# Kernel tuning notes

Measured on AMD Instinct MI355X. Metric: run time of the kernel, lower is better.

## Reference

```python
import jax, jax.numpy as jnp
import numpy as np

B, T, W, HP = 1, 64, 88, 48   # batch, frames, pitches, hidden_per_pitch
NU, NH, K = 24, 4, 25          # n_unit, n_heads, neighborhood window
HD = NU // NH                  # head dim = 6
HL = NU // 2                   # LSTM hidden per direction = 12


def _lstm_bidir(x, w_ih, w_hh, b_ih, b_hh):
    # x: [N, T, In]; w_ih: [2, 4*HL, In]; w_hh: [2, 4*HL, HL]; biases: [2, 4*HL]
    N = x.shape[0]
    def run(Wih, Whh, bih, bhh, reverse):
        def step(carry, xt):
            h, c = carry
            g = xt @ Wih.T + h @ Whh.T + bih + bhh
            i, f, gg, o = jnp.split(g, 4, axis=-1)  # torch gate order i,f,g,o
            c = jax.nn.sigmoid(f) * c + jax.nn.sigmoid(i) * jnp.tanh(gg)
            h = jax.nn.sigmoid(o) * jnp.tanh(c)
            return (h, c), h
        init = (jnp.zeros((N, HL), x.dtype), jnp.zeros((N, HL), x.dtype))
        _, ys = jax.lax.scan(step, init, jnp.swapaxes(x, 0, 1), reverse=reverse)
        return jnp.swapaxes(ys, 0, 1)
    return jnp.concatenate([run(w_ih[0], w_hh[0], b_ih[0], b_hh[0], False),
                            run(w_ih[1], w_hh[1], b_ih[1], b_hh[1], True)], axis=-1)


def _natten2d(x, qkv_w, qkv_b, rpb, proj_w, proj_b):
    # Neighborhood attention over 2D grid [B, Hh, Ww] with KxK window clamped at borders.
    Bn, Hh, Ww, C = x.shape
    qkv = (x @ qkv_w.T + qkv_b).reshape(Bn, Hh, Ww, 3, NH, HD)
    q = qkv[..., 0, :, :] * (HD ** -0.5)
    k = qkv[..., 1, :, :]
    v = qkv[..., 2, :, :]
    half = K // 2
    ar = jnp.arange(K)
    idx_i = jnp.clip(jnp.arange(Hh) - half, 0, Hh - K)[:, None] + ar  # [Hh,K]
    idx_j = jnp.clip(jnp.arange(Ww) - half, 0, Ww - K)[:, None] + ar  # [Ww,K]
    kg = k[:, idx_i][:, :, :, idx_j]  # [B,Hh,K,Ww,K,NH,HD]
    vg = v[:, idx_i][:, :, :, idx_j]
    ri = idx_i - jnp.arange(Hh)[:, None] + (K - 1)  # relative pos bias indices [Hh,K]
    rj = idx_j - jnp.arange(Ww)[:, None] + (K - 1)  # [Ww,K]
    bias = rpb[:, ri][:, :, :, rj]                  # [NH,Hh,K,Ww,K]
    logits = jnp.einsum('bijnd,biajcnd->bnijac', q, kg)
    logits = logits + jnp.transpose(bias, (0, 1, 3, 2, 4))[None]
    attn = jax.nn.softmax(logits.reshape(Bn, NH, Hh, Ww, K * K), axis=-1)
    attn = attn.reshape(Bn, NH, Hh, Ww, K, K)
    out = jnp.einsum('bnijac,biajcnd->bijnd', attn, vg).reshape(Bn, Hh, Ww, C)
    return out @ proj_w.T + proj_b


def _forward(features, condition, mask, emb, w_ih_l0, w_hh_l0, b_ih_l0, b_hh_l0,
             w_ih_l1, w_hh_l1, b_ih_l1, b_hh_l1, qkv_w, qkv_b, rpb, proj_w, proj_b,
             out_w, out_b):
    # concat: [B,T,88,HP] + [B,T,88,4] + [B,T,88,1] -> [B,T,88,HP+5]
    cat = jnp.concatenate([jnp.transpose(features, (0, 1, 3, 2)), emb[condition],
                           mask[..., None]], axis=-1)
    x = jnp.transpose(cat, (0, 2, 1, 3)).reshape(B * W, T, HP + 5)  # pitchwise LSTM
    x = _lstm_bidir(x, w_ih_l0, w_hh_l0, b_ih_l0, b_hh_l0)
    x = _lstm_bidir(x, w_ih_l1, w_hh_l1, b_ih_l1, b_hh_l1)
    x = jnp.transpose(x.reshape(B, W, T, NU), (0, 2, 1, 3))  # [B,T,88,NU]
    for _ in range(2):  # n_layers=2; Sequential(*[m]*2) => SHARED weights
        x = _natten2d(x, qkv_w, qkv_b, rpb, proj_w, proj_b)
    return x @ out_w.T + out_b  # [B,T,88,5]


def setup_inputs():
    ks = jax.random.split(jax.random.key(0), 24)
    def unif(k, shape, fan):
        s = 1.0 / np.sqrt(fan)
        return jax.random.uniform(k, shape, jnp.float32, -s, s)
    return {
        'features': jax.random.normal(ks[0], (B, T, HP, W), jnp.float32),
        'condition': jax.random.randint(ks[1], (B, T, W), 0, 5),
        'mask': jax.random.uniform(ks[2], (B, T, W), jnp.float32),
        'emb': jax.random.normal(ks[3], (5, 4), jnp.float32),
        'w_ih_l0': unif(ks[4], (2, 4 * HL, HP + 5), HL),
        'w_hh_l0': unif(ks[5], (2, 4 * HL, HL), HL),
        'b_ih_l0': unif(ks[6], (2, 4 * HL), HL),
        'b_hh_l0': unif(ks[7], (2, 4 * HL), HL),
        'w_ih_l1': unif(ks[8], (2, 4 * HL, 2 * HL), HL),
        'w_hh_l1': unif(ks[9], (2, 4 * HL, HL), HL),
        'b_ih_l1': unif(ks[10], (2, 4 * HL), HL),
        'b_hh_l1': unif(ks[11], (2, 4 * HL), HL),
        'qkv_w': unif(ks[12], (3 * NU, NU), NU),
        'qkv_b': unif(ks[13], (3 * NU,), NU),
        'rpb': jax.random.normal(ks[14], (NH, 2 * K - 1, 2 * K - 1), jnp.float32) * 0.02,
        'proj_w': unif(ks[15], (NU, NU), NU),
        'proj_b': unif(ks[16], (NU,), NU),
        'out_w': unif(ks[17], (5, NU), NU),
        'out_b': unif(ks[18], (5,), NU),
    }


def reference(features, condition, mask, emb, w_ih_l0, w_hh_l0, b_ih_l0, b_hh_l0,
              w_ih_l1, w_hh_l1, b_ih_l1, b_hh_l1, qkv_w, qkv_b, rpb, proj_w, proj_b,
              out_w, out_b):
    return _forward(features, condition, mask, emb, w_ih_l0, w_hh_l0, b_ih_l0, b_hh_l0,
                    w_ih_l1, w_hh_l1, b_ih_l1, b_hh_l1, qkv_w, qkv_b, rpb,
                    proj_w, proj_b, out_w, out_b)
```

## Files before the change

### kernel.cpp

```cpp
#include <hip/hip_runtime.h>
#include <hip/hip_bf16.h>

#define NPIX (64*88)
#define NSEQ 88
#define TT 64
#define F0 53
#define GATES 48

typedef __hip_bfloat16 bf16;

__device__ __forceinline__ float frcp(float x){ return __builtin_amdgcn_rcpf(x); }
__device__ __forceinline__ float blo(unsigned u){ return __uint_as_float(u<<16); }
__device__ __forceinline__ float bhi(unsigned u){ return __uint_as_float(u & 0xffff0000u); }

__global__ __launch_bounds__(1024) void k_core(
    const float* __restrict__ feat, const int* __restrict__ cond,
    const float* __restrict__ mask, const float* __restrict__ emb,
    const float* __restrict__ wih0, const float* __restrict__ whh0,
    const float* __restrict__ bih0, const float* __restrict__ bhh0,
    const float* __restrict__ wih1, const float* __restrict__ whh1,
    const float* __restrict__ bih1, const float* __restrict__ bhh1,
    const float* __restrict__ qkv_w, const float* __restrict__ qkv_b,
    float* __restrict__ q, bf16* __restrict__ kh, bf16* __restrict__ vh){
  int n = (blockIdx.x & 7)*11 + (blockIdx.x >> 3);
  int tid = threadIdx.x;
  int wave = tid >> 6; int lane = tid & 63;
  __shared__ float smem[14816];
  float* gbuf = smem;
  float* sx   = smem + 6144;
  float* sw0  = smem + 6144+3392;
  float* w1   = smem + 6144;
  float* sqkv = smem + 6144+2400;
  float* y0   = smem + 6144+4200;
  float* y1   = smem + 6144+5736;
  float* bsum = smem + 14624;

  for (int idx = tid; idx < 2*GATES*F0; idx += 1024) sw0[idx] = wih0[idx];
  for (int idx = tid; idx < TT*F0; idx += 1024){
    int t = idx / F0, f = idx - t*F0;
    float v;
    if (f < 48)      v = feat[(t*48 + f)*88 + n];
    else if (f < 52) v = emb[cond[t*88+n]*4 + (f-48)];
    else             v = mask[t*88+n];
    sx[idx] = v;
  }
  if (tid < 96)       bsum[tid] = bih0[tid] + bhh0[tid];
  else if (tid < 192) bsum[tid] = bih1[tid-96] + bhh1[tid-96];
  __syncthreads();

  #pragma unroll
  for (int r = 0; r < 6; ++r){
    int row = tid + r*1024;
    int d = row / 3072; int rem = row - d*3072;
    int t = rem / 48; int j = rem - t*48;
    const float* xr = sx + t*F0;
    const float* wr = sw0 + (d*GATES + j)*F0;
    float a0=0.f, a1=0.f, a2=0.f, a3=0.f;
    #pragma unroll
    for (int f=0; f<52; f+=4){
      a0 += xr[f  ]*wr[f  ];
      a1 += xr[f+1]*wr[f+1];
      a2 += xr[f+2]*wr[f+2];
      a3 += xr[f+3]*wr[f+3];
    }
    gbuf[(d*TT + t)*GATES + j] = bsum[d*GATES+j] + xr[52]*wr[52] + ((a0+a1)+(a2+a3));
  }
  __syncthreads();

  if (wave >= 2){
    for (int idx = tid-128; idx < 2*GATES*24; idx += 896){
      int row = idx / 24, f = idx - row*24;
      w1[row*25 + f] = wih1[idx];
    }
    for (int idx = tid-128; idx < 72*24; idx += 896){
      int row = idx / 24, f = idx - row*24;
      sqkv[row*25 + f] = qkv_w[idx];
    }
  } else {
    int d = wave;
    int j = (lane < GATES) ? lane : (lane - GATES);
    int u = j % 12; int grp = j / 12;
    float w[12];
    const float* wb = whh0 + (d*GATES + j)*12;
    #pragma unroll
    for (int m=0;m<12;++m) w[m] = wb[m];
    float negs  = (grp==2) ? -2.f : -1.f;
    float amul  = (grp==2) ?  2.f :  1.f;
    float aadd  = (grp==2) ? -1.f :  0.f;
    const float* gb = gbuf + d*TT*GATES + j;
    float hval = 0.f, cval = 0.f;
    int t0 = d ? (TT-1) : 0;
    float gnext = gb[t0*GATES];
    for (int s=0;s<TT;++s){
      int t = d ? (TT-1-s) : s;
      float gg = gnext;
      int tn = d ? max(TT-2-s,0) : min(s+1,TT-1);
      gnext = gb[tn*GATES];
      float h0=__shfl(hval,0), h1=__shfl(hval,1), h2=__shfl(hval,2);
      float h3=__shfl(hval,3), h4=__shfl(hval,4), h5=__shfl(hval,5);
      float h6=__shfl(hval,6), h7=__shfl(hval,7), h8=__shfl(hval,8);
      float h9=__shfl(hval,9), h10=__shfl(hval,10), h11=__shfl(hval,11);
      float a0 = gg + h0*w[0] + h4*w[4] + h8*w[8];
      float a1 = h1*w[1] + h5*w[5] + h9*w[9];
      float a2 = h2*w[2] + h6*w[6] + h10*w[10];
      float a3 = h3*w[3] + h7*w[7] + h11*w[11];
      float dot = (a0+a1)+(a2+a3);
      float act = amul*frcp(1.f + __expf(negs*dot)) + aadd;
      float ai = __shfl(act, u);
      float af = __shfl(act, u+12);
      float ag = __shfl(act, u+24);
      float ao = __shfl(act, u+36);
      float cn = af*cval + ai*ag;
      float th = 2.f*frcp(1.f + __expf(-2.f*cn)) - 1.f;
      hval = ao*th; cval = cn;
      if (lane < 12) y0[t*24 + d*12 + lane] = hval;
    }
  }
  __syncthreads();

  #pragma unroll
  for (int r = 0; r < 6; ++r){
    int row = tid + r*1024;
    int d = row / 3072; int rem = row - d*3072;
    int t = rem / 48; int j = rem - t*48;
    const float* xr = y0 + t*24;
    const float* wr = w1 + (d*GATES + j)*25;
    float a0=0.f, a1=0.f;
    #pragma unroll
    for (int c=0; c<24; c+=2){ a0 += xr[c]*wr[c]; a1 += xr[c+1]*wr[c+1]; }
    gbuf[(d*TT + t)*GATES + j] = bsum[96 + d*GATES+j] + a0 + a1;
  }
  __syncthreads();

  if (wave < 2){
    int d = wave;
    int j = (lane < GATES) ? lane : (lane - GATES);
    int u = j % 12; int grp = j / 12;
    float w[12];
    const float* wb = whh1 + (d*GATES + j)*12;
    #pragma unroll
    for (int m=0;m<12;++m) w[m] = wb[m];
    float negs  = (grp==2) ? -2.f : -1.f;
    float amul  = (grp==2) ?  2.f :  1.f;
    float aadd  = (grp==2) ? -1.f :  0.f;
    const float* gb = gbuf + d*TT*GATES + j;
    float hval = 0.f, cval = 0.f;
    int t0 = d ? (TT-1) : 0;
    float gnext = gb[t0*GATES];
    for (int s=0;s<TT;++s){
      int t = d ? (TT-1-s) : s;
      float gg = gnext;
      int tn = d ? max(TT-2-s,0) : min(s+1,TT-1);
      gnext = gb[tn*GATES];
      float h0=__shfl(hval,0), h1=__shfl(hval,1), h2=__shfl(hval,2);
      float h3=__shfl(hval,3), h4=__shfl(hval,4), h5=__shfl(hval,5);
      float h6=__shfl(hval,6), h7=__shfl(hval,7), h8=__shfl(hval,8);
      float h9=__shfl(hval,9), h10=__shfl(hval,10), h11=__shfl(hval,11);
      float a0 = gg + h0*w[0] + h4*w[4] + h8*w[8];
      float a1 = h1*w[1] + h5*w[5] + h9*w[9];
      float a2 = h2*w[2] + h6*w[6] + h10*w[10];
      float a3 = h3*w[3] + h7*w[7] + h11*w[11];
      float dot = (a0+a1)+(a2+a3);
      float act = amul*frcp(1.f + __expf(negs*dot)) + aadd;
      float ai = __shfl(act, u);
      float af = __shfl(act, u+12);
      float ag = __shfl(act, u+24);
      float ao = __shfl(act, u+36);
      float cn = af*cval + ai*ag;
      float th = 2.f*frcp(1.f + __expf(-2.f*cn)) - 1.f;
      hval = ao*th; cval = cn;
      if (lane < 12) y1[t*24 + d*12 + lane] = hval;
    }
  }
  __syncthreads();

  for (int idx = tid; idx < TT*72; idx += 1024){
    int gq = idx % 72; int t = idx / 72;
    int p = t*88 + n;
    const float* xr = y1 + t*24;
    const float* wr = sqkv + gq*25;
    float a0=0.f, a1=0.f;
    #pragma unroll
    for (int c=0; c<24; c+=2){ a0 += xr[c]*wr[c]; a1 += xr[c+1]*wr[c+1]; }
    float acc = qkv_b[gq] + a0 + a1;
    int s = gq/24, rem = gq - s*24;
    if (s==0) q[p*24+rem] = acc*0.4082482904638631f;
    else {
      int hh = rem/6, pos = rem - hh*6;
      bf16* dst = (s==1) ? kh : vh;
      dst[((size_t)hh*NPIX + p)*8 + pos] = __float2bfloat16(acc);
    }
  }
}

__global__ __launch_bounds__(512) void k_attn(
    const float* __restrict__ q, const bf16* __restrict__ kh,
    const bf16* __restrict__ vh, const float* __restrict__ rpb,
    float* __restrict__ ao){
  int b = blockIdx.x;
  int h = b / 704; int rem = b - h*704;
  int ti = rem / 44, tj = rem - ti*44;
  int i0 = ti*4, j0 = tj*2;
  int tid = threadIdx.x;
  int w = tid >> 6; int lane = tid & 63;
  int osi = min(max(i0-12,0),39);
  int osj = min(max(j0-12,0),63);

  __shared__ unsigned kt[728*5];
  __shared__ unsigned vt[728*5];
  const uint4* kg = (const uint4*)(kh + (size_t)h*NPIX*8);
  const uint4* vg = (const uint4*)(vh + (size_t)h*NPIX*8);
  for (int idx = tid; idx < 728; idx += 512){
    int a = idx / 26, cc = idx - a*26;
    int gi = min(osi + a, 63), gj = min(osj + cc, 87);
    int src = gi*88 + gj;
    uint4 kr = kg[src];
    uint4 vr = vg[src];
    int o = idx*5;
    kt[o] = kr.x; kt[o+1] = kr.y; kt[o+2] = kr.z;
    vt[o] = vr.x; vt[o+1] = vr.y; vt[o+2] = vr.z;
  }
  __syncthreads();

  int pi = i0 + (w>>1), pj = j0 + (w&1);
  int p = pi*88 + pj;
  int dsi = min(max(pi-12,0),39) - osi;
  int dsj = min(max(pj-12,0),63) - osj;
  int rbi = osi + dsi - pi + 24;
  int rbj = osj + dsj - pj + 24;

  float qv[6];
  #pragma unroll
  for (int d=0; d<6; ++d) qv[d] = q[p*24 + h*6 + d];

  float lgv[10]; int rof[10];
  float lmax = -1e30f;
  #pragma unroll
  for (int it=0; it<10; ++it){
    int nb = lane + it*64;
    bool valid = nb < 625;
    int nbc = valid ? nb : 624;
    int a = nbc/25, cc = nbc - a*25;
    int r5 = ((a+dsi)*26 + (cc+dsj))*5;
    rof[it] = r5;
    unsigned k0 = kt[r5], k1 = kt[r5+1], k2 = kt[r5+2];
    float lg = qv[0]*blo(k0)+qv[1]*bhi(k0)+qv[2]*blo(k1)
             + qv[3]*bhi(k1)+qv[4]*blo(k2)+qv[5]*bhi(k2);
    lg += rpb[(h*49 + (a + rbi))*49 + (cc + rbj)];
    lg = valid ? lg : -1e30f;
    lgv[it] = lg;
    lmax = fmaxf(lmax, lg);
  }
  #pragma unroll
  for (int off=32; off; off>>=1) lmax = fmaxf(lmax, __shfl_xor(lmax, off));
  float lsum = 0.f;
  #pragma unroll
  for (int it=0; it<10; ++it){
    float pe = __expf(lgv[it]-lmax);
    lgv[it] = pe; lsum += pe;
  }
  #pragma unroll
  for (int off=32; off; off>>=1) lsum += __shfl_xor(lsum, off);
  float acc[6] = {0,0,0,0,0,0};
  #pragma unroll
  for (int it=0; it<10; ++it){
    int r5 = rof[it];
    unsigned v0 = vt[r5], v1 = vt[r5+1], v2 = vt[r5+2];
    float pe = lgv[it];
    acc[0] += pe*blo(v0); acc[1] += pe*bhi(v0);
    acc[2] += pe*blo(v1); acc[3] += pe*bhi(v1);
    acc[4] += pe*blo(v2); acc[5] += pe*bhi(v2);
  }
  #pragma unroll
  for (int d=0; d<6; ++d){
    #pragma unroll
    for (int off=32; off; off>>=1) acc[d] += __shfl_xor(acc[d], off);
  }
  if (lane == 0){
    float inv = frcp(lsum);
    #pragma unroll
    for (int d=0; d<6; ++d) ao[p*24 + h*6 + d] = acc[d]*inv;
  }
}

__global__ __launch_bounds__(64) void k_proj_qkv(const float* __restrict__ ain,
    const float* __restrict__ pw, const float* __restrict__ pb,
    const float* __restrict__ qkv_w, const float* __restrict__ qkv_b,
    float* __restrict__ q2, bf16* __restrict__ kh2, bf16* __restrict__ vh2){
  int p = blockIdx.x; int tid = threadIdx.x;
  __shared__ float arow[24];
  __shared__ float xrow[24];
  if (tid < 24) arow[tid] = ain[p*24+tid];
  __syncthreads();
  if (tid < 24){
    float a2 = pb[tid];
    const float* wr = pw + tid*24;
    #pragma unroll
    for (int c=0;c<24;++c) a2 += arow[c]*wr[c];
    xrow[tid] = a2;
  }
  __syncthreads();
  for (int g = tid; g < 72; g += 64){
    float a2 = qkv_b[g];
    const float* wr = qkv_w + g*24;
    #pragma unroll
    for (int c=0;c<24;++c) a2 += xrow[c]*wr[c];
    int s = g/24, rem = g - s*24;
    if (s==0) q2[p*24+rem] = a2*0.4082482904638631f;
    else {
      int hh = rem/6, pos = rem - hh*6;
      bf16* dst = (s==1) ? kh2 : vh2;
      dst[((size_t)hh*NPIX + p)*8 + pos] = __float2bfloat16(a2);
    }
  }
}

__global__ __launch_bounds__(64) void k_proj_out(const float* __restrict__ ain,
    const float* __restrict__ pw, const float* __restrict__ pb,
    const float* __restrict__ ow, const float* __restrict__ ob,
    float* __restrict__ out){
  int p = blockIdx.x; int tid = threadIdx.x;
  __shared__ float arow[24];
  __shared__ float xrow[24];
  if (tid < 24) arow[tid] = ain[p*24+tid];
  __syncthreads();
  if (tid < 24){
    float a2 = pb[tid];
    const float* wr = pw + tid*24;
    #pragma unroll
    for (int c=0;c<24;++c) a2 += arow[c]*wr[c];
    xrow[tid] = a2;
  }
  __syncthreads();
  if (tid < 5){
    float a2 = ob[tid];
    const float* wr = ow + tid*24;
    #pragma unroll
    for (int c=0;c<24;++c) a2 += xrow[c]*wr[c];
    out[p*5+tid] = a2;
  }
}

extern "C" void kernel_launch(void* const* d_in, const int* in_sizes, int n_in,
                              void* d_out, int out_size, void* d_ws, size_t ws_size,
                              hipStream_t stream) {
  const float* feat    = (const float*)d_in[0];
  const int*   cond    = (const int*)  d_in[1];
  const float* mask    = (const float*)d_in[2];
  const float* emb     = (const float*)d_in[3];
  const float* w_ih_l0 = (const float*)d_in[4];
  const float* w_hh_l0 = (const float*)d_in[5];
  const float* b_ih_l0 = (const float*)d_in[6];
  const float* b_hh_l0 = (const float*)d_in[7];
  const float* w_ih_l1 = (const float*)d_in[8];
  const float* w_hh_l1 = (const float*)d_in[9];
  const float* b_ih_l1 = (const float*)d_in[10];
  const float* b_hh_l1 = (const float*)d_in[11];
  const float* qkv_w   = (const float*)d_in[12];
  const float* qkv_b   = (const float*)d_in[13];
  const float* rpb     = (const float*)d_in[14];
  const float* proj_w  = (const float*)d_in[15];
  const float* proj_b  = (const float*)d_in[16];
  const float* out_w   = (const float*)d_in[17];
  const float* out_b   = (const float*)d_in[18];
  float* out = (float*)d_out;

  float* ws  = (float*)d_ws;
  float* Q1  = ws;
  float* Q2  = Q1 + 135168;
  float* AO  = Q2 + 135168;
  bf16*  KH1 = (bf16*)(AO + 135168);
  bf16*  VH1 = KH1 + 180224;
  bf16*  KH2 = VH1 + 180224;
  bf16*  VH2 = KH2 + 180224;

  k_core<<<NSEQ, 1024, 0, stream>>>(
      feat, cond, mask, emb,
      w_ih_l0, w_hh_l0, b_ih_l0, b_hh_l0,
      w_ih_l1, w_hh_l1, b_ih_l1, b_hh_l1,
      qkv_w, qkv_b, Q1, KH1, VH1);

  k_attn<<<4*16*44, 512, 0, stream>>>(Q1, KH1, VH1, rpb, AO);

  k_proj_qkv<<<NPIX, 64, 0, stream>>>(AO, proj_w, proj_b, qkv_w, qkv_b,
                                      Q2, KH2, VH2);

  k_attn<<<4*16*44, 512, 0, stream>>>(Q2, KH2, VH2, rpb, AO);

  k_proj_out<<<NPIX, 64, 0, stream>>>(AO, proj_w, proj_b, out_w, out_b, out);
}
```

Baseline: 207.6 us.

## Fuse first attention pass with projection and QKV into per-pixel kernel

```diff
diff --git a/kernel.cpp b/kernel.cpp
--- a/kernel.cpp
+++ b/kernel.cpp
@@ -12,6 +12,15 @@
 __device__ __forceinline__ float frcp(float x){ return __builtin_amdgcn_rcpf(x); }
 __device__ __forceinline__ float blo(unsigned u){ return __uint_as_float(u<<16); }
 __device__ __forceinline__ float bhi(unsigned u){ return __uint_as_float(u & 0xffff0000u); }
+
+__device__ __forceinline__ void unpack6(uint4 r, float* f){
+  f[0] = __uint_as_float(r.x << 16);
+  f[1] = __uint_as_float(r.x & 0xffff0000u);
+  f[2] = __uint_as_float(r.y << 16);
+  f[3] = __uint_as_float(r.y & 0xffff0000u);
+  f[4] = __uint_as_float(r.z << 16);
+  f[5] = __uint_as_float(r.z & 0xffff0000u);
+}
 
 __global__ __launch_bounds__(1024) void k_core(
     const float* __restrict__ feat, const int* __restrict__ cond,
@@ -193,6 +202,98 @@
   }
 }
 
+__global__ __launch_bounds__(256) void k_attn1(
+    const float* __restrict__ q, const bf16* __restrict__ kh,
+    const bf16* __restrict__ vh, const float* __restrict__ rpb,
+    const float* __restrict__ pw, const float* __restrict__ pb,
+    const float* __restrict__ qkv_w, const float* __restrict__ qkv_b,
+    float* __restrict__ q2, bf16* __restrict__ kh2, bf16* __restrict__ vh2){
+  int p = blockIdx.x; int tid = threadIdx.x;
+  int h = tid >> 6; int lane = tid & 63;
+  int i = p / 88, j = p - i*88;
+  int si = min(max(i-12,0),39), sj = min(max(j-12,0),63);
+  __shared__ float aorow[24];
+  __shared__ float xrow[24];
+
+  float qv[6];
+  #pragma unroll
+  for (int d=0; d<6; ++d) qv[d] = q[p*24 + h*6 + d];
+  const uint4* kb = (const uint4*)(kh + (size_t)h*NPIX*8);
+  const uint4* vb = (const uint4*)(vh + (size_t)h*NPIX*8);
+  float lgv[10]; int roff[10];
+  float lmax = -1e30f;
+  #pragma unroll
+  for (int it=0; it<10; ++it){
+    int nb = lane + it*64;
+    bool valid = nb < 625;
+    int nbc = valid ? nb : 624;
+    int a = nbc/25, cc = nbc - a*25;
+    int gi = si + a, gj = sj + cc;
+    int row = gi*88+gj;
+    roff[it] = row;
+    float kr[6];
+    unpack6(kb[row], kr);
+    float lg = qv[0]*kr[0]+qv[1]*kr[1]+qv[2]*kr[2]+qv[3]*kr[3]+qv[4]*kr[4]+qv[5]*kr[5];
+    lg += rpb[(h*49 + (gi - i + 24))*49 + (gj - j + 24)];
+    lg = valid ? lg : -1e30f;
+    lgv[it] = lg;
+    lmax = fmaxf(lmax, lg);
+  }
+  #pragma unroll
+  for (int off=32; off; off>>=1) lmax = fmaxf(lmax, __shfl_xor(lmax, off));
+  float lsum = 0.f;
+  #pragma unroll
+  for (int it=0; it<10; ++it){
+    float pe = __expf(lgv[it]-lmax);
+    lgv[it] = pe; lsum += pe;
+  }
+  #pragma unroll
+  for (int off=32; off; off>>=1) lsum += __shfl_xor(lsum, off);
+  float acc[6] = {0,0,0,0,0,0};
+  #pragma unroll
+  for (int it=0; it<10; ++it){
+    float vr[6];
+    unpack6(vb[roff[it]], vr);
+    float pe = lgv[it];
+    #pragma unroll
+    for (int d=0; d<6; ++d) acc[d] += pe*vr[d];
+  }
+  #pragma unroll
+  for (int d=0; d<6; ++d){
+    #pragma unroll
+    for (int off=32; off; off>>=1) acc[d] += __shfl_xor(acc[d], off);
+  }
+  if (lane == 0){
+    float inv = frcp(lsum);
+    #pragma unroll
+    for (int d=0; d<6; ++d) aorow[h*6+d] = acc[d]*inv;
+  }
+  __syncthreads();
+
+  if (tid < 24){
+    float a2 = pb[tid];
+    const float* wr = pw + tid*24;
+    #pragma unroll
+    for (int c=0;c<24;++c) a2 += aorow[c]*wr[c];
+    xrow[tid] = a2;
+  }
+  __syncthreads();
+
+  if (tid < 72){
+    float a2 = qkv_b[tid];
+    const float* wr = qkv_w + tid*24;
+    #pragma unroll
+    for (int c=0;c<24;++c) a2 += xrow[c]*wr[c];
+    int s = tid/24, rem = tid - s*24;
+    if (s==0) q2[p*24+rem] = a2*0.4082482904638631f;
+    else {
+      int hh = rem/6, pos = rem - hh*6;
+      bf16* dst = (s==1) ? kh2 : vh2;
+      dst[((size_t)hh*NPIX + p)*8 + pos] = __float2bfloat16(a2);
+    }
+  }
+}
+
 __global__ __launch_bounds__(512) void k_attn(
     const float* __restrict__ q, const bf16* __restrict__ kh,
     const bf16* __restrict__ vh, const float* __restrict__ rpb,
@@ -280,38 +381,6 @@
     float inv = frcp(lsum);
     #pragma unroll
     for (int d=0; d<6; ++d) ao[p*24 + h*6 + d] = acc[d]*inv;
-  }
-}
-
-__global__ __launch_bounds__(64) void k_proj_qkv(const float* __restrict__ ain,
-    const float* __restrict__ pw, const float* __restrict__ pb,
-    const float* __restrict__ qkv_w, const float* __restrict__ qkv_b,
-    float* __restrict__ q2, bf16* __restrict__ kh2, bf16* __restrict__ vh2){
-  int p = blockIdx.x; int tid = threadIdx.x;
-  __shared__ float arow[24];
-  __shared__ float xrow[24];
-  if (tid < 24) arow[tid] = ain[p*24+tid];
-  __syncthreads();
-  if (tid < 24){
-    float a2 = pb[tid];
-    const float* wr = pw + tid*24;
-    #pragma unroll
-    for (int c=0;c<24;++c) a2 += arow[c]*wr[c];
-    xrow[tid] = a2;
-  }
-  __syncthreads();
-  for (int g = tid; g < 72; g += 64){
-    float a2 = qkv_b[g];
-    const float* wr = qkv_w + g*24;
-    #pragma unroll
-    for (int c=0;c<24;++c) a2 += xrow[c]*wr[c];
-    int s = g/24, rem = g - s*24;
-    if (s==0) q2[p*24+rem] = a2*0.4082482904638631f;
-    else {
-      int hh = rem/6, pos = rem - hh*6;
-      bf16* dst = (s==1) ? kh2 : vh2;
-      dst[((size_t)hh*NPIX + p)*8 + pos] = __float2bfloat16(a2);
-    }
   }
 }
 
@@ -380,10 +449,9 @@
       w_ih_l1, w_hh_l1, b_ih_l1, b_hh_l1,
       qkv_w, qkv_b, Q1, KH1, VH1);
 
-  k_attn<<<4*16*44, 512, 0, stream>>>(Q1, KH1, VH1, rpb, AO);
-
-  k_proj_qkv<<<NPIX, 64, 0, stream>>>(AO, proj_w, proj_b, qkv_w, qkv_b,
-                                      Q2, KH2, VH2);
+  k_attn1<<<NPIX, 256, 0, stream>>>(
+      Q1, KH1, VH1, rpb, proj_w, proj_b, qkv_w, qkv_b,
+      Q2, KH2, VH2);
 
   k_attn<<<4*16*44, 512, 0, stream>>>(Q2, KH2, VH2, rpb, AO);
 
```

After: 204.6 us. Within noise of the previous version (-1.5%).
